# Optimization experiments

Hardware: AMD Instinct MI355X
Metric: run time of the kernel (lower is better)

The kernel has to match this reference:

```python
import jax, jax.numpy as jnp
import numpy as np

B, S, T, K = 128, 4, 16, 36   # questions, answer slots (hardcoded 4), max tags/slot, num boxes
VD, QD, H = 256, 256, 256
NB = B * S * T                # total tag rows = leading dim of v, q


def setup_inputs() -> dict:
    key = jax.random.key(0)
    ks = jax.random.split(key, 8)
    tags_attention = jnp.ones((B, S, T), dtype=jnp.int32)  # all slots full -> sum == NB
    v = jax.random.normal(ks[0], (NB, K, VD), jnp.float32)
    q = jax.random.normal(ks[1], (NB, QD), jnp.float32)
    # binary box mask, first box always valid
    bm = (jax.random.uniform(ks[2], (B, K)) < 0.85).astype(jnp.float32)
    box_mask = bm.at[:, 0].set(1.0)
    Wv = jax.random.normal(ks[3], (H, VD), jnp.float32) / np.sqrt(VD).astype(np.float32)
    bv = jnp.zeros((H,), jnp.float32)
    Wq = jax.random.normal(ks[4], (H, QD), jnp.float32) / np.sqrt(QD).astype(np.float32)
    bq = jnp.zeros((H,), jnp.float32)
    Wl = jax.random.normal(ks[5], (1, H), jnp.float32) / np.sqrt(H).astype(np.float32)
    bl = jnp.zeros((1,), jnp.float32)
    return dict(v=v, q=q, box_mask=box_mask, tags_attention=tags_attention,
                Wv=Wv, bv=bv, Wq=Wq, bq=bq, Wl=Wl, bl=bl)


def reference(v, q, box_mask, tags_attention, Wv, bv, Wq, bq, Wl, bl):
    # FCNet projections (weight-normed Linear + ReLU; dropout inactive at eval)
    v_proj = jax.nn.relu(jnp.einsum('nkd,hd->nkh', v, Wv) + bv)          # [N,K,H]
    q_proj = jax.nn.relu(q @ Wq.T + bq)                                   # [N,H]
    joint = v_proj * q_proj[:, None, :]                                   # [N,K,H]
    logits = jnp.einsum('nkh,h->nk', joint, Wl[0]) + bl[0]                # [N,K]

    # pad_sequence: ragged rows -> [B,S,T,K] via per-slot offsets + masked gather
    Bq, Ss, Tt = tags_attention.shape
    lengths = tags_attention.sum(-1)                                      # [B,S]
    flat_len = lengths.reshape(-1)
    offsets = jnp.concatenate([jnp.zeros((1,), flat_len.dtype),
                               jnp.cumsum(flat_len)[:-1]]).reshape(Bq, Ss)
    t = jnp.arange(Tt)
    idx = offsets[:, :, None] + t                                         # [B,S,T]
    valid = t[None, None, :] < lengths[:, :, None]                        # [B,S,T]
    gathered = logits[jnp.clip(idx, 0, logits.shape[0] - 1)]              # [B,S,T,K]
    logits_batch = jnp.where(valid[..., None], gathered, 0.0)

    # masked_softmax (r2c style): softmax(x*mask)*mask, renormalized
    mask = box_mask[:, None, None, :]                                     # [B,1,1,K]
    w = jax.nn.softmax(logits_batch * mask, axis=-1) * mask
    w = w / (w.sum(-1, keepdims=True) + 1e-13)
    return w
```

## Files before the change

kernel.cpp:

```cpp
#include <hip/hip_runtime.h>
#include <hip/hip_bf16.h>
#include <stdint.h>

#define NBROWS 8192
#define KBOX   36
#define MROWS  (NBROWS * KBOX)

typedef __attribute__((ext_vector_type(8))) short bf16x8;
typedef __attribute__((ext_vector_type(4))) float f32x4;

__device__ __forceinline__ unsigned short f2bf(float f) {
  unsigned int u = __float_as_uint(f);
  return (unsigned short)((u + 0x7fffu + ((u >> 16) & 1u)) >> 16);
}

__device__ __forceinline__ unsigned int pk2(float x, float y) {
  __hip_bfloat16 hx = __float2bfloat16(x);
  __hip_bfloat16 hy = __float2bfloat16(y);
  unsigned short ux, uy;
  __builtin_memcpy(&ux, &hx, 2);
  __builtin_memcpy(&uy, &hy, 2);
  return (unsigned)ux | ((unsigned)uy << 16);
}

__device__ __forceinline__ void gll16(const void* g, void* l) {
  __builtin_amdgcn_global_load_lds((const __attribute__((address_space(1))) unsigned int*)g,
                                   (__attribute__((address_space(3))) unsigned int*)l,
                                   16, 0, 0);
}

__global__ void cvt_kernel(const float* __restrict__ Wv, const float* __restrict__ Wq,
                           unsigned short* __restrict__ wvb, unsigned short* __restrict__ wqb) {
  int i = blockIdx.x * 256 + threadIdx.x;
  wvb[i] = f2bf(Wv[i]);
  wqb[i] = f2bf(Wq[i]);
}

template<int MODE>
__global__ __launch_bounds__(256, 3)
void gemm_kernel(const float* __restrict__ Amat,
                 const unsigned short* __restrict__ Wbf,
                 const float* __restrict__ bias,
                 const float* __restrict__ wl,
                 const float* __restrict__ g,
                 float* __restrict__ outp,
                 const float* __restrict__ blp)
{
  __shared__ unsigned short Asm[2][64 * 32];
  __shared__ unsigned short Bsm[2][256 * 32];
  __shared__ float bias_sm[256];
  __shared__ float aux_sm[4 * 256];
  __shared__ float partial[64 * 4];

  const int t    = threadIdx.x;
  const int lane = t & 63;
  const int wid  = t >> 6;
  const int r0   = blockIdx.x * 64;

  bias_sm[t] = bias[t];
  int n_base = 0;
  if (MODE == 0) {
    aux_sm[t] = wl[t];
  } else {
    n_base = r0 / KBOX;
    #pragma unroll
    for (int i = 0; i < 4; ++i) {
      int idx = t + i * 256;
      int n = n_base + (idx >> 8);
      if (n > NBROWS - 1) n = NBROWS - 1;
      aux_sm[idx] = g[(size_t)n * 256 + (idx & 255)];
    }
  }

  int bh[4], bco[4];
  #pragma unroll
  for (int i = 0; i < 4; ++i) {
    int h = wid * 64 + i * 16 + (lane >> 2);
    bh[i]  = h;
    bco[i] = ((lane & 3) ^ ((h >> 1) & 3)) * 8;
  }

  const int arow = t >> 2;
  const int ako  = t & 3;
  const float* asrc = Amat + (size_t)(r0 + arow) * 256 + ako * 8;
  const int adst_off = arow * 32 + (ako ^ ((arow >> 1) & 3)) * 8;

  f32x4 acc[4][4];
  #pragma unroll
  for (int a = 0; a < 4; ++a)
    #pragma unroll
    for (int b = 0; b < 4; ++b) acc[a][b] = (f32x4)0.f;

  float4 areg[2][2];

  #pragma unroll
  for (int i = 0; i < 4; ++i)
    gll16(Wbf + (size_t)bh[i] * 256 + bco[i], &Bsm[0][(wid * 64 + i * 16) * 32]);
  areg[0][0] = ((const float4*)(asrc + 0))[0];
  areg[0][1] = ((const float4*)(asrc + 0))[1];
  areg[1][0] = ((const float4*)(asrc + 32))[0];
  areg[1][1] = ((const float4*)(asrc + 32))[1];
  {
    uint4 pk;
    pk.x = pk2(areg[0][0].x, areg[0][0].y);
    pk.y = pk2(areg[0][0].z, areg[0][0].w);
    pk.z = pk2(areg[0][1].x, areg[0][1].y);
    pk.w = pk2(areg[0][1].z, areg[0][1].w);
    *(uint4*)&Asm[0][adst_off] = pk;
  }
  __syncthreads();

  #pragma unroll
  for (int kk = 0; kk < 8; ++kk) {
    const int cur = kk & 1;
    if (kk < 7) {
      const int d0 = (kk + 1) * 32;
      #pragma unroll
      for (int i = 0; i < 4; ++i)
        gll16(Wbf + (size_t)bh[i] * 256 + d0 + bco[i], &Bsm[1 - cur][(wid * 64 + i * 16) * 32]);
      const float4 a0 = areg[(kk + 1) & 1][0];
      const float4 a1 = areg[(kk + 1) & 1][1];
      uint4 pk;
      pk.x = pk2(a0.x, a0.y);
      pk.y = pk2(a0.z, a0.w);
      pk.z = pk2(a1.x, a1.y);
      pk.w = pk2(a1.z, a1.w);
      *(uint4*)&Asm[1 - cur][adst_off] = pk;
    }
    if (kk < 6) {
      const int d0 = (kk + 2) * 32;
      areg[kk & 1][0] = ((const float4*)(asrc + d0))[0];
      areg[kk & 1][1] = ((const float4*)(asrc + d0))[1];
    }
    bf16x8 af[4], bfr[4];
    #pragma unroll
    for (int mf = 0; mf < 4; ++mf) {
      int row  = mf * 16 + (lane & 15);
      int phys = (lane >> 4) ^ ((row >> 1) & 3);
      af[mf] = *(const bf16x8*)&Asm[cur][row * 32 + phys * 8];
    }
    #pragma unroll
    for (int nf = 0; nf < 4; ++nf) {
      int col  = wid * 64 + nf * 16 + (lane & 15);
      int phys = (lane >> 4) ^ ((col >> 1) & 3);
      bfr[nf] = *(const bf16x8*)&Bsm[cur][col * 32 + phys * 8];
    }
    #pragma unroll
    for (int mf = 0; mf < 4; ++mf)
      #pragma unroll
      for (int nf = 0; nf < 4; ++nf)
        acc[mf][nf] = __builtin_amdgcn_mfma_f32_16x16x32_bf16(af[mf], bfr[nf], acc[mf][nf], 0, 0, 0);
    __syncthreads();
  }

  if (MODE == 0) {
    #pragma unroll
    for (int mf = 0; mf < 4; ++mf)
      #pragma unroll
      for (int nf = 0; nf < 4; ++nf) {
        int col = wid * 64 + nf * 16 + (lane & 15);
        float bb = bias_sm[col];
        float ww = aux_sm[col];
        #pragma unroll
        for (int j = 0; j < 4; ++j) {
          int row = mf * 16 + ((lane >> 4) << 2) + j;
          float x = fmaxf(acc[mf][nf][j] + bb, 0.f) * ww;
          outp[(size_t)(r0 + row) * 256 + col] = x;
        }
      }
  } else {
    float s[4][4];
    #pragma unroll
    for (int mf = 0; mf < 4; ++mf) {
      #pragma unroll
      for (int j = 0; j < 4; ++j) {
        int row  = mf * 16 + ((lane >> 4) << 2) + j;
        int nloc = (r0 + row) / KBOX - n_base;
        const float* grow = &aux_sm[nloc * 256];
        float acc_s = 0.f;
        #pragma unroll
        for (int nf = 0; nf < 4; ++nf) {
          int col = wid * 64 + nf * 16 + (lane & 15);
          float x = acc[mf][nf][j] + bias_sm[col];
          acc_s += fmaxf(x, 0.f) * grow[col];
        }
        s[mf][j] = acc_s;
      }
    }
    #pragma unroll
    for (int mf = 0; mf < 4; ++mf)
      #pragma unroll
      for (int j = 0; j < 4; ++j) {
        float vv = s[mf][j];
        vv += __shfl_xor(vv, 1);
        vv += __shfl_xor(vv, 2);
        vv += __shfl_xor(vv, 4);
        vv += __shfl_xor(vv, 8);
        s[mf][j] = vv;
      }
    if ((lane & 15) == 0) {
      #pragma unroll
      for (int mf = 0; mf < 4; ++mf)
        #pragma unroll
        for (int j = 0; j < 4; ++j) {
          int row = mf * 16 + ((lane >> 4) << 2) + j;
          partial[row * 4 + wid] = s[mf][j];
        }
    }
    __syncthreads();
    if (t < 64) {
      float vv = partial[t * 4 + 0] + partial[t * 4 + 1] + partial[t * 4 + 2] + partial[t * 4 + 3];
      outp[r0 + t] = vv + blp[0];
    }
  }
}

__global__ __launch_bounds__(256)
void softmax_kernel(const float* __restrict__ logits, const float* __restrict__ box_mask,
                    float* __restrict__ outp) {
  int n = blockIdx.x * 4 + (threadIdx.x >> 6);
  int k = threadIdx.x & 63;
  int b = n >> 6;
  float l = 0.f, m = 0.f;
  if (k < KBOX) {
    m = box_mask[b * KBOX + k];
    l = logits[(size_t)n * KBOX + k];
  }
  bool act = (k < KBOX) && (m > 0.5f);
  float lm = act ? l : -3.0e38f;
  #pragma unroll
  for (int off = 32; off >= 1; off >>= 1) lm = fmaxf(lm, __shfl_xor(lm, off));
  float e = act ? expf(l - lm) : 0.f;
  float ssum = e;
  #pragma unroll
  for (int off = 32; off >= 1; off >>= 1) ssum += __shfl_xor(ssum, off);
  if (k < KBOX) outp[(size_t)n * KBOX + k] = e / ssum;
}

extern "C" void kernel_launch(void* const* d_in, const int* in_sizes, int n_in,
                              void* d_out, int out_size, void* d_ws, size_t ws_size,
                              hipStream_t stream) {
  const float* v        = (const float*)d_in[0];
  const float* q        = (const float*)d_in[1];
  const float* box_mask = (const float*)d_in[2];
  const float* Wv = (const float*)d_in[4];
  const float* bv = (const float*)d_in[5];
  const float* Wq = (const float*)d_in[6];
  const float* bq = (const float*)d_in[7];
  const float* Wl = (const float*)d_in[8];
  const float* bl = (const float*)d_in[9];
  float* outp = (float*)d_out;

  char* ws = (char*)d_ws;
  unsigned short* wvb = (unsigned short*)ws;
  unsigned short* wqb = (unsigned short*)(ws + 131072);
  float* g      = (float*)(ws + 262144);
  float* logits = (float*)(ws + 262144 + 8388608);

  cvt_kernel<<<256, 256, 0, stream>>>(Wv, Wq, wvb, wqb);
  gemm_kernel<0><<<NBROWS / 64, 256, 0, stream>>>(q, wqb, bq, Wl, nullptr, g, nullptr);
  gemm_kernel<1><<<MROWS / 64, 256, 0, stream>>>(v, wvb, bv, nullptr, g, logits, bl);
  softmax_kernel<<<NBROWS / 4, 256, 0, stream>>>(logits, box_mask, outp);
}
```

Before: 121.6 us.

## Stage weight tiles through registers and write LDS after MFMAs with lighter barrier

Replaces the direct global-to-LDS loads of the bf16 weight tile with register-staged loads. The LDS stores for both A and B tiles now come after the MFMA block, so global load latency overlaps with compute. The full __syncthreads is swapped for an lgkmcnt wait plus s_barrier, and the final iteration's barrier is dropped. Occupancy hint drops from 3 to 2 blocks per SM to make room for the extra staging registers, which may reduce latency hiding.

```diff
diff --git a/kernel.cpp b/kernel.cpp
--- a/kernel.cpp
+++ b/kernel.cpp
@@ -23,11 +23,10 @@
   return (unsigned)ux | ((unsigned)uy << 16);
 }
 
-__device__ __forceinline__ void gll16(const void* g, void* l) {
-  __builtin_amdgcn_global_load_lds((const __attribute__((address_space(1))) unsigned int*)g,
-                                   (__attribute__((address_space(3))) unsigned int*)l,
-                                   16, 0, 0);
-}
+#define LGKM_BARRIER() do {                                   \
+    asm volatile("s_waitcnt lgkmcnt(0)" ::: "memory");        \
+    asm volatile("s_barrier" ::: "memory");                   \
+  } while (0)
 
 __global__ void cvt_kernel(const float* __restrict__ Wv, const float* __restrict__ Wq,
                            unsigned short* __restrict__ wvb, unsigned short* __restrict__ wqb) {
@@ -37,7 +36,7 @@
 }
 
 template<int MODE>
-__global__ __launch_bounds__(256, 3)
+__global__ __launch_bounds__(256, 2)
 void gemm_kernel(const float* __restrict__ Amat,
                  const unsigned short* __restrict__ Wbf,
                  const float* __restrict__ bias,
@@ -72,14 +71,8 @@
     }
   }
 
-  int bh[4], bco[4];
-  #pragma unroll
-  for (int i = 0; i < 4; ++i) {
-    int h = wid * 64 + i * 16 + (lane >> 2);
-    bh[i]  = h;
-    bco[i] = ((lane & 3) ^ ((h >> 1) & 3)) * 8;
-  }
-
+  const int brow = t >> 2;
+  const int bko  = t & 3;
   const int arow = t >> 2;
   const int ako  = t & 3;
   const float* asrc = Amat + (size_t)(r0 + arow) * 256 + ako * 8;
@@ -91,24 +84,30 @@
     #pragma unroll
     for (int b = 0; b < 4; ++b) acc[a][b] = (f32x4)0.f;
 
-  float4 areg[2][2];
+  float4 aregA[2], aregB[2];
+  uint4  breg[4];
 
   #pragma unroll
   for (int i = 0; i < 4; ++i)
-    gll16(Wbf + (size_t)bh[i] * 256 + bco[i], &Bsm[0][(wid * 64 + i * 16) * 32]);
-  areg[0][0] = ((const float4*)(asrc + 0))[0];
-  areg[0][1] = ((const float4*)(asrc + 0))[1];
-  areg[1][0] = ((const float4*)(asrc + 32))[0];
-  areg[1][1] = ((const float4*)(asrc + 32))[1];
+    breg[i] = *(const uint4*)&Wbf[(brow + i * 64) * 256 + 0 + bko * 8];
+  aregA[0] = ((const float4*)(asrc + 0))[0];
+  aregA[1] = ((const float4*)(asrc + 0))[1];
+  aregB[0] = ((const float4*)(asrc + 32))[0];
+  aregB[1] = ((const float4*)(asrc + 32))[1];
+  #pragma unroll
+  for (int i = 0; i < 4; ++i) {
+    int r = brow + i * 64;
+    *(uint4*)&Bsm[0][r * 32 + (bko ^ ((r >> 1) & 3)) * 8] = breg[i];
+  }
   {
     uint4 pk;
-    pk.x = pk2(areg[0][0].x, areg[0][0].y);
-    pk.y = pk2(areg[0][0].z, areg[0][0].w);
-    pk.z = pk2(areg[0][1].x, areg[0][1].y);
-    pk.w = pk2(areg[0][1].z, areg[0][1].w);
+    pk.x = pk2(aregA[0].x, aregA[0].y);
+    pk.y = pk2(aregA[0].z, aregA[0].w);
+    pk.z = pk2(aregA[1].x, aregA[1].y);
+    pk.w = pk2(aregA[1].z, aregA[1].w);
     *(uint4*)&Asm[0][adst_off] = pk;
   }
-  __syncthreads();
+  LGKM_BARRIER();
 
   #pragma unroll
   for (int kk = 0; kk < 8; ++kk) {
@@ -117,40 +116,49 @@
       const int d0 = (kk + 1) * 32;
       #pragma unroll
       for (int i = 0; i < 4; ++i)
-        gll16(Wbf + (size_t)bh[i] * 256 + d0 + bco[i], &Bsm[1 - cur][(wid * 64 + i * 16) * 32]);
-      const float4 a0 = areg[(kk + 1) & 1][0];
-      const float4 a1 = areg[(kk + 1) & 1][1];
+        breg[i] = *(const uint4*)&Wbf[(brow + i * 64) * 256 + d0 + bko * 8];
+    }
+    if (kk < 6) {
+      const int d0 = (kk + 2) * 32;
+      float4 t0 = ((const float4*)(asrc + d0))[0];
+      float4 t1 = ((const float4*)(asrc + d0))[1];
+      if (kk & 1) { aregB[0] = t0; aregB[1] = t1; }
+      else        { aregA[0] = t0; aregA[1] = t1; }
+    }
+    bf16x8 af[4], bfr[4];
+    #pragma unroll
+    for (int mf = 0; mf < 4; ++mf) {
+      int row  = mf * 16 + (lane & 15);
+      int phys = (lane >> 4) ^ ((row >> 1) & 3);
+      af[mf] = *(const bf16x8*)&Asm[cur][row * 32 + phys * 8];
+    }
+    #pragma unroll
+    for (int nf = 0; nf < 4; ++nf) {
+      int col  = wid * 64 + nf * 16 + (lane & 15);
+      int phys = (lane >> 4) ^ ((col >> 1) & 3);
+      bfr[nf] = *(const bf16x8*)&Bsm[cur][col * 32 + phys * 8];
+    }
+    #pragma unroll
+    for (int mf = 0; mf < 4; ++mf)
+      #pragma unroll
+      for (int nf = 0; nf < 4; ++nf)
+        acc[mf][nf] = __builtin_amdgcn_mfma_f32_16x16x32_bf16(af[mf], bfr[nf], acc[mf][nf], 0, 0, 0);
+    if (kk < 7) {
+      #pragma unroll
+      for (int i = 0; i < 4; ++i) {
+        int r = brow + i * 64;
+        *(uint4*)&Bsm[1 - cur][r * 32 + (bko ^ ((r >> 1) & 3)) * 8] = breg[i];
+      }
+      const float4 a0 = (kk & 1) ? aregA[0] : aregB[0];
+      const float4 a1 = (kk & 1) ? aregA[1] : aregB[1];
       uint4 pk;
       pk.x = pk2(a0.x, a0.y);
       pk.y = pk2(a0.z, a0.w);
       pk.z = pk2(a1.x, a1.y);
       pk.w = pk2(a1.z, a1.w);
       *(uint4*)&Asm[1 - cur][adst_off] = pk;
-    }
-    if (kk < 6) {
-      const int d0 = (kk + 2) * 32;
-      areg[kk & 1][0] = ((const float4*)(asrc + d0))[0];
-      areg[kk & 1][1] = ((const float4*)(asrc + d0))[1];
-    }
-    bf16x8 af[4], bfr[4];
-    #pragma unroll
-    for (int mf = 0; mf < 4; ++mf) {
-      int row  = mf * 16 + (lane & 15);
-      int phys = (lane >> 4) ^ ((row >> 1) & 3);
-      af[mf] = *(const bf16x8*)&Asm[cur][row * 32 + phys * 8];
-    }
-    #pragma unroll
-    for (int nf = 0; nf < 4; ++nf) {
-      int col  = wid * 64 + nf * 16 + (lane & 15);
-      int phys = (lane >> 4) ^ ((col >> 1) & 3);
-      bfr[nf] = *(const bf16x8*)&Bsm[cur][col * 32 + phys * 8];
-    }
-    #pragma unroll
-    for (int mf = 0; mf < 4; ++mf)
-      #pragma unroll
-      for (int nf = 0; nf < 4; ++nf)
-        acc[mf][nf] = __builtin_amdgcn_mfma_f32_16x16x32_bf16(af[mf], bfr[nf], acc[mf][nf], 0, 0, 0);
-    __syncthreads();
+      LGKM_BARRIER();
+    }
   }
 
   if (MODE == 0) {
```

Result: faster. 116.1 us (-4.5%).
